# Kernel optimization log

Hardware: AMD Instinct MI355X
Metric: run time of the kernel (lower is better)

## Reference

```python
import jax, jax.numpy as jnp
import numpy as np

B, S, D, H, F = 4, 2048, 512, 8, 2048
HD = D // H
SCALE = HD ** -0.5


def layernorm(x, g, b, eps=1e-5):
    mu = jnp.mean(x, axis=-1, keepdims=True)
    var = jnp.var(x, axis=-1, keepdims=True)
    return (x - mu) * jax.lax.rsqrt(var + eps) * g + b


def setup_inputs() -> dict:
    key = jax.random.key(0)
    ks = jax.random.split(key, 10)
    s = 0.02
    return {
        "x": jax.random.normal(ks[0], (B, S, D), jnp.float32),
        "w_qkv": jax.random.normal(ks[1], (D, 3 * D), jnp.float32) * s,
        "b_qkv": jnp.zeros((3 * D,), jnp.float32),
        "w_o": jax.random.normal(ks[2], (D, D), jnp.float32) * s,
        "b_o": jnp.zeros((D,), jnp.float32),
        "w1": jax.random.normal(ks[3], (D, F), jnp.float32) * s,
        "b1": jnp.zeros((F,), jnp.float32),
        "w2": jax.random.normal(ks[4], (F, D), jnp.float32) * s,
        "b2": jnp.zeros((D,), jnp.float32),
        "g1": jnp.ones((D,), jnp.float32),
        "be1": jnp.zeros((D,), jnp.float32),
        "g2": jnp.ones((D,), jnp.float32),
        "be2": jnp.zeros((D,), jnp.float32),
    }


def reference(x, w_qkv, b_qkv, w_o, b_o, w1, b1, w2, b2, g1, be1, g2, be2):
    res = x
    qkv = x @ w_qkv + b_qkv                       # [B,S,3D]
    q, k, v = jnp.split(qkv, 3, axis=-1)          # each [B,S,D]
    # head partition: [B,S,D] -> [B,H,S,hd]
    def split_heads(t):
        return t.reshape(B, S, H, HD).transpose(0, 2, 1, 3)
    q, k, v = map(split_heads, (q, k, v))
    scores = jnp.einsum('bhqc,bhkc->bhqk', q, k) * SCALE
    weights = jax.nn.softmax(scores, axis=-1)
    out = jnp.einsum('bhqk,bhkc->bhqc', weights, v)
    out = out.transpose(0, 2, 1, 3).reshape(B, S, D)  # merge heads
    out = out @ w_o + b_o
    out = layernorm(out + res, g1, be1)
    res = out
    out = jax.nn.gelu(out @ w1 + b1, approximate=False) @ w2 + b2
    out = layernorm(out + res, g2, be2)
    return out
```

## Files before the change

### kernel.cpp

```cpp
#include <hip/hip_runtime.h>
#include <math.h>

constexpr int B = 4, S = 2048, D = 512, H = 8, HD = 64, F = 2048;
constexpr int M = B * S;
constexpr float C_QK = 0.125f * 1.44269504088896340736f;

typedef __bf16 bf16x8 __attribute__((ext_vector_type(8)));
typedef float  f32x4  __attribute__((ext_vector_type(4)));
typedef float  f32x16 __attribute__((ext_vector_type(16)));

static __device__ __forceinline__ short f2bf(float f) {
  return __builtin_bit_cast(short, (__bf16)f);
}

static __device__ __forceinline__ void gload16(const void* g, void* l) {
  __builtin_amdgcn_global_load_lds(
      (const __attribute__((address_space(1))) unsigned int*)g,
      (__attribute__((address_space(3))) unsigned int*)l, 16, 0, 0);
}

__global__ __launch_bounds__(256)
void cast_x(const float4* __restrict__ in, short4* __restrict__ out) {
  int i = blockIdx.x * 256 + threadIdx.x;
  float4 v = in[i];
  out[i] = make_short4(f2bf(v.x), f2bf(v.y), f2bf(v.z), f2bf(v.w));
}

__global__ __launch_bounds__(256)
void tcast(const float* __restrict__ in, short* __restrict__ out, int R, int C) {
  __shared__ float tl[32][33];
  const int t = threadIdx.x;
  const int r0 = blockIdx.y * 32, c0 = blockIdx.x * 32;
  const int tr = t >> 3, tc4 = (t & 7) * 4;
  float4 v = *(const float4*)&in[(size_t)(r0 + tr) * C + c0 + tc4];
  tl[tr][tc4] = v.x; tl[tr][tc4 + 1] = v.y; tl[tr][tc4 + 2] = v.z; tl[tr][tc4 + 3] = v.w;
  __syncthreads();
  short4 o = make_short4(f2bf(tl[tc4][tr]), f2bf(tl[tc4 + 1][tr]),
                         f2bf(tl[tc4 + 2][tr]), f2bf(tl[tc4 + 3][tr]));
  *(short4*)&out[(size_t)(c0 + tr) * R + r0 + tc4] = o;
}

template<int BM, int GELU, int EPI>
__global__ __launch_bounds__(256)
void gemm_bf16(const short* __restrict__ A, const short* __restrict__ Wt,
               const float* __restrict__ bias,
               float* __restrict__ Cf, short* __restrict__ Cb,
               short* __restrict__ qsw, short* __restrict__ ksw,
               short* __restrict__ vsw, int K, int N) {
  constexpr int MI = BM / 32;
  __shared__ short As[BM * 32] __attribute__((aligned(16)));
  __shared__ short Bs[128 * 32] __attribute__((aligned(16)));
  const int t = threadIdx.x;
  const int w = t >> 6, l = t & 63, g = l >> 4, r = l & 15;
  const int wm = w >> 1, wn = w & 1;
  const int m0 = blockIdx.y * BM, n0 = blockIdx.x * 128;
  f32x4 acc[MI][4] = {};
  for (int k0 = 0; k0 < K; k0 += 32) {
    __syncthreads();
#pragma unroll
    for (int iss = 0; iss < BM / 64; ++iss) {
      int q = iss * 256 + t;
      gload16(A + (size_t)(m0 + (q >> 2)) * K + k0 + (q & 3) * 8, (char*)As + q * 16);
    }
#pragma unroll
    for (int iss = 0; iss < 2; ++iss) {
      int q = iss * 256 + t;
      gload16(Wt + (size_t)(n0 + (q >> 2)) * K + k0 + (q & 3) * 8, (char*)Bs + q * 16);
    }
    __syncthreads();
    bf16x8 aF[MI], bF[4];
#pragma unroll
    for (int mi = 0; mi < MI; ++mi)
      aF[mi] = *(const bf16x8*)(As + (wm * (MI * 16) + mi * 16 + r) * 32 + g * 8);
#pragma unroll
    for (int ni = 0; ni < 4; ++ni)
      bF[ni] = *(const bf16x8*)(Bs + (wn * 64 + ni * 16 + r) * 32 + g * 8);
#pragma unroll
    for (int mi = 0; mi < MI; ++mi)
#pragma unroll
      for (int ni = 0; ni < 4; ++ni)
        acc[mi][ni] = __builtin_amdgcn_mfma_f32_16x16x32_bf16(aF[mi], bF[ni], acc[mi][ni], 0, 0, 0);
  }
#pragma unroll
  for (int mi = 0; mi < MI; ++mi) {
#pragma unroll
    for (int ni = 0; ni < 4; ++ni) {
      const int n  = n0 + wn * 64 + ni * 16 + r;
      const int mB = m0 + wm * (MI * 16) + mi * 16 + g * 4;
      float vals[4];
#pragma unroll
      for (int j = 0; j < 4; ++j) {
        float v = acc[mi][ni][j] + bias[n];
        if (GELU) v = 0.5f * v * (1.0f + erff(v * 0.70710678118654752f));
        vals[j] = v;
      }
      if (EPI == 0) {
#pragma unroll
        for (int j = 0; j < 4; ++j) Cf[(size_t)(mB + j) * N + n] = vals[j];
      } else if (EPI == 1) {
#pragma unroll
        for (int j = 0; j < 4; ++j) Cb[(size_t)(mB + j) * N + n] = f2bf(vals[j]);
      } else {
        const int b = mB >> 11, s = mB & 2047;
        if (n < 512) {
          const int hh = n >> 6, d = n & 63;
          const size_t rb = (size_t)(b * 8 + hh) * 2048;
#pragma unroll
          for (int j = 0; j < 4; ++j)
            qsw[(rb + s + j) * 64 + (d ^ (((s + j) & 7) << 3))] = f2bf(vals[j] * C_QK);
        } else if (n < 1024) {
          const int hh = (n - 512) >> 6, d = (n - 512) & 63;
          const size_t rb = (size_t)(b * 8 + hh) * 2048;
#pragma unroll
          for (int j = 0; j < 4; ++j)
            ksw[(rb + s + j) * 64 + (d ^ (((s + j) & 7) << 3))] = f2bf(vals[j]);
        } else {
          const int hh = (n - 1024) >> 6, d = (n - 1024) & 63;
          short4 pk = make_short4(f2bf(vals[0]), f2bf(vals[1]), f2bf(vals[2]), f2bf(vals[3]));
          *(short4*)&vsw[(size_t)((b * 8 + hh) * 64 + d) * 2048 + (s ^ ((d & 7) << 3))] = pk;
        }
      }
    }
  }
}

__global__ __launch_bounds__(256)
void attn_mfma(const short* __restrict__ qsw, const short* __restrict__ ksw,
               const short* __restrict__ vsw, short* __restrict__ attn_o) {
  __shared__ short Qs[128 * 64] __attribute__((aligned(16)));
  __shared__ short Ks[64 * 64] __attribute__((aligned(16)));
  __shared__ short Vs[64 * 64] __attribute__((aligned(16)));
  const int t = threadIdx.x;
  const int w = t >> 6, l = t & 63;
  const int c = l & 31, hi = l >> 5;
  const int bh = blockIdx.y;
  const int q0 = blockIdx.x * 128;
  const short* qb = qsw + ((size_t)bh * 2048 + q0) * 64;
  const short* kb = ksw + (size_t)bh * 2048 * 64;
  const short* vb = vsw + (size_t)bh * 64 * 2048;

#pragma unroll
  for (int iss = 0; iss < 4; ++iss) {
    int q = iss * 256 + t;
    gload16(qb + (q >> 3) * 64 + (q & 7) * 8, (char*)Qs + q * 16);
  }
  __syncthreads();
  const int qrow = w * 32 + c;
  const int swz = (c & 7) << 3;
  bf16x8 qf[4];
#pragma unroll
  for (int dc = 0; dc < 4; ++dc)
    qf[dc] = *(const bf16x8*)(Qs + qrow * 64 + ((dc * 16 + hi * 8) ^ swz));

  f32x16 o0 = {}, o1 = {};
  float m_run = -3e38f, l_run = 0.0f;

  for (int kt = 0; kt < S; kt += 64) {
    __syncthreads();
#pragma unroll
    for (int iss = 0; iss < 2; ++iss) {
      int q = iss * 256 + t;
      gload16(kb + (size_t)(kt + (q >> 3)) * 64 + (q & 7) * 8, (char*)Ks + q * 16);
    }
#pragma unroll
    for (int iss = 0; iss < 2; ++iss) {
      int q = iss * 256 + t;
      gload16(vb + (size_t)(q >> 3) * 2048 + kt + (q & 7) * 8, (char*)Vs + q * 16);
    }
    __syncthreads();

    f32x16 s0 = {}, s1 = {};
#pragma unroll
    for (int dc = 0; dc < 4; ++dc) {
      const int koff = (dc * 16 + hi * 8) ^ swz;
      bf16x8 kf0 = *(const bf16x8*)(Ks + c * 64 + koff);
      bf16x8 kf1 = *(const bf16x8*)(Ks + (32 + c) * 64 + koff);
      s0 = __builtin_amdgcn_mfma_f32_32x32x16_bf16(kf0, qf[dc], s0, 0, 0, 0);
      s1 = __builtin_amdgcn_mfma_f32_32x32x16_bf16(kf1, qf[dc], s1, 0, 0, 0);
    }
    float tmax = -3e38f;
#pragma unroll
    for (int j = 0; j < 16; ++j) tmax = fmaxf(tmax, fmaxf(s0[j], s1[j]));
    tmax = fmaxf(tmax, __shfl_xor(tmax, 32, 64));
    if (__any(tmax - m_run > 8.0f)) {
      float mnew = fmaxf(m_run, tmax);
      float rs = __builtin_amdgcn_exp2f(m_run - mnew);
      m_run = mnew;
      l_run *= rs;
#pragma unroll
      for (int j = 0; j < 16; ++j) {
        float rj = __shfl(rs, (j & 3) + 8 * (j >> 2) + 4 * hi, 64);
        o0[j] *= rj; o1[j] *= rj;
      }
    }
    float rsum = 0.0f;
#pragma unroll
    for (int j = 0; j < 16; ++j) {
      s0[j] = __builtin_amdgcn_exp2f(s0[j] - m_run);
      s1[j] = __builtin_amdgcn_exp2f(s1[j] - m_run);
      rsum += s0[j] + s1[j];
    }
    rsum += __shfl_xor(rsum, 32, 64);
    l_run += rsum;

#pragma unroll
    for (int kc = 0; kc < 4; ++kc) {
      const int jb = (kc & 1) * 8;
      int u0, u1, v0, v1;
      if (kc < 2) {
        asm("v_cvt_pk_bf16_f32 %0, %1, %2" : "=v"(u0) : "v"(s0[jb + 0]), "v"(s0[jb + 1]));
        asm("v_cvt_pk_bf16_f32 %0, %1, %2" : "=v"(u1) : "v"(s0[jb + 2]), "v"(s0[jb + 3]));
        asm("v_cvt_pk_bf16_f32 %0, %1, %2" : "=v"(v0) : "v"(s0[jb + 4]), "v"(s0[jb + 5]));
        asm("v_cvt_pk_bf16_f32 %0, %1, %2" : "=v"(v1) : "v"(s0[jb + 6]), "v"(s0[jb + 7]));
      } else {
        asm("v_cvt_pk_bf16_f32 %0, %1, %2" : "=v"(u0) : "v"(s1[jb + 0]), "v"(s1[jb + 1]));
        asm("v_cvt_pk_bf16_f32 %0, %1, %2" : "=v"(u1) : "v"(s1[jb + 2]), "v"(s1[jb + 3]));
        asm("v_cvt_pk_bf16_f32 %0, %1, %2" : "=v"(v0) : "v"(s1[jb + 4]), "v"(s1[jb + 5]));
        asm("v_cvt_pk_bf16_f32 %0, %1, %2" : "=v"(v1) : "v"(s1[jb + 6]), "v"(s1[jb + 7]));
      }
      asm volatile("v_permlane32_swap_b32 %0, %1" : "+v"(u0), "+v"(v0));
      asm volatile("v_permlane32_swap_b32 %0, %1" : "+v"(u1), "+v"(v1));
      int pw[4] = {u0, u1, v0, v1};
      bf16x8 pa = __builtin_bit_cast(bf16x8, *(int4*)pw);
      const int voff = (kc * 16 + hi * 8) ^ swz;
      bf16x8 vf0 = *(const bf16x8*)(Vs + c * 64 + voff);
      bf16x8 vf1 = *(const bf16x8*)(Vs + (32 + c) * 64 + voff);
      o0 = __builtin_amdgcn_mfma_f32_32x32x16_bf16(pa, vf0, o0, 0, 0, 0);
      o1 = __builtin_amdgcn_mfma_f32_32x32x16_bf16(pa, vf1, o1, 0, 0, 0);
    }
  }
  const int b = bh >> 3, hh = bh & 7;
  float inv = 1.0f / l_run;
#pragma unroll
  for (int j = 0; j < 16; ++j) {
    const int q_rel = (j & 3) + 8 * (j >> 2) + 4 * hi;
    float invq = __shfl(inv, q_rel, 64);
    const size_t row = (size_t)(b * 2048 + q0 + w * 32 + q_rel) * 512 + hh * 64;
    attn_o[row + c]      = f2bf(o0[j] * invq);
    attn_o[row + 32 + c] = f2bf(o1[j] * invq);
  }
}

template<int WB>
__global__ __launch_bounds__(256)
void add_ln(const float* __restrict__ a, const float* __restrict__ res,
            const float* __restrict__ g_, const float* __restrict__ be,
            float* __restrict__ out, short* __restrict__ outb) {
  const int row = blockIdx.x;
  const int t = threadIdx.x;
  const size_t off = (size_t)row * D;
  float x0 = a[off + t] + res[off + t];
  float x1 = a[off + t + 256] + res[off + t + 256];
  float sum = x0 + x1;
  float sq  = x0 * x0 + x1 * x1;
#pragma unroll
  for (int o2 = 32; o2 > 0; o2 >>= 1) {
    sum += __shfl_down(sum, o2);
    sq  += __shfl_down(sq, o2);
  }
  __shared__ float ssum[4], ssq[4];
  const int wid = t >> 6;
  if ((t & 63) == 0) { ssum[wid] = sum; ssq[wid] = sq; }
  __syncthreads();
  if (t == 0) {
    ssum[0] = ssum[0] + ssum[1] + ssum[2] + ssum[3];
    ssq[0]  = ssq[0] + ssq[1] + ssq[2] + ssq[3];
  }
  __syncthreads();
  float mu   = ssum[0] * (1.0f / D);
  float var  = ssq[0] * (1.0f / D) - mu * mu;
  float rstd = rsqrtf(var + 1e-5f);
  float y0 = (x0 - mu) * rstd * g_[t] + be[t];
  float y1 = (x1 - mu) * rstd * g_[t + 256] + be[t + 256];
  out[off + t] = y0;
  out[off + t + 256] = y1;
  if (WB) {
    outb[off + t] = f2bf(y0);
    outb[off + t + 256] = f2bf(y1);
  }
}

extern "C" void kernel_launch(void* const* d_in, const int* in_sizes, int n_in,
                              void* d_out, int out_size, void* d_ws, size_t ws_size,
                              hipStream_t stream) {
  const float* x     = (const float*)d_in[0];
  const float* w_qkv = (const float*)d_in[1];
  const float* b_qkv = (const float*)d_in[2];
  const float* w_o   = (const float*)d_in[3];
  const float* b_o   = (const float*)d_in[4];
  const float* w1    = (const float*)d_in[5];
  const float* b1    = (const float*)d_in[6];
  const float* w2    = (const float*)d_in[7];
  const float* b2    = (const float*)d_in[8];
  const float* g1    = (const float*)d_in[9];
  const float* be1   = (const float*)d_in[10];
  const float* g2    = (const float*)d_in[11];
  const float* be2   = (const float*)d_in[12];
  float* out = (float*)d_out;
  (void)in_sizes; (void)n_in; (void)out_size; (void)ws_size;

  const size_t MD = (size_t)M * 512;
  short* q_sw = (short*)d_ws;
  short* k_sw = q_sw + MD;
  short* v_sw = k_sw + MD;
  short* a_o  = v_sw + MD;
  short* h    = q_sw;
  short* xb   = a_o + MD;
  short* ln1b = xb;
  short* wtq  = xb + MD;
  short* wto  = wtq + (size_t)1536 * 512;
  short* wt1  = wto + (size_t)512 * 512;
  short* wt2  = wt1 + (size_t)512 * 2048;
  float* buf  = (float*)(wt2 + (size_t)2048 * 512);
  float* ln1  = buf + MD;

  cast_x<<<4096, 256, 0, stream>>>((const float4*)x, (short4*)xb);
  tcast<<<dim3(48, 16), 256, 0, stream>>>(w_qkv, wtq, 512, 1536);
  tcast<<<dim3(16, 16), 256, 0, stream>>>(w_o,  wto, 512, 512);
  tcast<<<dim3(64, 16), 256, 0, stream>>>(w1,   wt1, 512, 2048);
  tcast<<<dim3(16, 64), 256, 0, stream>>>(w2,   wt2, 2048, 512);

  gemm_bf16<128, 0, 2><<<dim3(12, 64), 256, 0, stream>>>(
      xb, wtq, b_qkv, nullptr, nullptr, q_sw, k_sw, v_sw, 512, 1536);
  attn_mfma<<<dim3(16, 32), 256, 0, stream>>>(q_sw, k_sw, v_sw, a_o);
  gemm_bf16<128, 0, 0><<<dim3(4, 64), 256, 0, stream>>>(
      a_o, wto, b_o, buf, nullptr, nullptr, nullptr, nullptr, 512, 512);
  add_ln<1><<<M, 256, 0, stream>>>(buf, x, g1, be1, ln1, ln1b);
  gemm_bf16<128, 1, 1><<<dim3(16, 64), 256, 0, stream>>>(
      ln1b, wt1, b1, nullptr, h, nullptr, nullptr, nullptr, 512, 2048);
  gemm_bf16<128, 0, 0><<<dim3(4, 64), 256, 0, stream>>>(
      h, wt2, b2, buf, nullptr, nullptr, nullptr, nullptr, 2048, 512);
  add_ln<0><<<M, 256, 0, stream>>>(buf, ln1, g2, be2, out, nullptr);
}
```

Measured before the change: 305.7 us.

## Double-buffer GEMM and attention LDS tiles, fuse prep casts into one kernel

```diff
diff --git a/kernel.cpp b/kernel.cpp
--- a/kernel.cpp
+++ b/kernel.cpp
@@ -20,17 +20,26 @@
 }
 
 __global__ __launch_bounds__(256)
-void cast_x(const float4* __restrict__ in, short4* __restrict__ out) {
-  int i = blockIdx.x * 256 + threadIdx.x;
-  float4 v = in[i];
-  out[i] = make_short4(f2bf(v.x), f2bf(v.y), f2bf(v.z), f2bf(v.w));
-}
-
-__global__ __launch_bounds__(256)
-void tcast(const float* __restrict__ in, short* __restrict__ out, int R, int C) {
+void prep_all(const float* __restrict__ x, short* __restrict__ xb,
+              const float* __restrict__ w_qkv, short* __restrict__ wtq,
+              const float* __restrict__ w_o,  short* __restrict__ wto,
+              const float* __restrict__ w1,   short* __restrict__ wt1,
+              const float* __restrict__ w2,   short* __restrict__ wt2) {
   __shared__ float tl[32][33];
+  const int id = blockIdx.x;
   const int t = threadIdx.x;
-  const int r0 = blockIdx.y * 32, c0 = blockIdx.x * 32;
+  if (id < 4096) {
+    int i = id * 256 + t;
+    float4 v = ((const float4*)x)[i];
+    ((short4*)xb)[i] = make_short4(f2bf(v.x), f2bf(v.y), f2bf(v.z), f2bf(v.w));
+    return;
+  }
+  const float* in; short* out; int R, C, bx, by;
+  if (id < 4864)      { int k = id - 4096; in = w_qkv; out = wtq; R = 512;  C = 1536; bx = k % 48; by = k / 48; }
+  else if (id < 5120) { int k = id - 4864; in = w_o;   out = wto; R = 512;  C = 512;  bx = k % 16; by = k / 16; }
+  else if (id < 6144) { int k = id - 5120; in = w1;    out = wt1; R = 512;  C = 2048; bx = k % 64; by = k / 64; }
+  else                { int k = id - 6144; in = w2;    out = wt2; R = 2048; C = 512;  bx = k % 16; by = k / 16; }
+  const int r0 = by * 32, c0 = bx * 32;
   const int tr = t >> 3, tc4 = (t & 7) * 4;
   float4 v = *(const float4*)&in[(size_t)(r0 + tr) * C + c0 + tc4];
   tl[tr][tc4] = v.x; tl[tr][tc4 + 1] = v.y; tl[tr][tc4 + 2] = v.z; tl[tr][tc4 + 3] = v.w;
@@ -40,53 +49,77 @@
   *(short4*)&out[(size_t)(c0 + tr) * R + r0 + tc4] = o;
 }
 
-template<int BM, int GELU, int EPI>
+template<int GELU, int EPI>
 __global__ __launch_bounds__(256)
 void gemm_bf16(const short* __restrict__ A, const short* __restrict__ Wt,
                const float* __restrict__ bias,
                float* __restrict__ Cf, short* __restrict__ Cb,
                short* __restrict__ qsw, short* __restrict__ ksw,
                short* __restrict__ vsw, int K, int N) {
-  constexpr int MI = BM / 32;
-  __shared__ short As[BM * 32] __attribute__((aligned(16)));
-  __shared__ short Bs[128 * 32] __attribute__((aligned(16)));
+  __shared__ short As[2][128 * 64] __attribute__((aligned(16)));
+  __shared__ short Bs[2][128 * 64] __attribute__((aligned(16)));
   const int t = threadIdx.x;
   const int w = t >> 6, l = t & 63, g = l >> 4, r = l & 15;
   const int wm = w >> 1, wn = w & 1;
-  const int m0 = blockIdx.y * BM, n0 = blockIdx.x * 128;
-  f32x4 acc[MI][4] = {};
-  for (int k0 = 0; k0 < K; k0 += 32) {
+  const int m0 = blockIdx.y * 128, n0 = blockIdx.x * 128;
+
+#define STAGE_TILE(buf, k0)                                                     \
+  {                                                                             \
+    _Pragma("unroll")                                                           \
+    for (int iss = 0; iss < 4; ++iss) {                                         \
+      int q = iss * 256 + t;                                                    \
+      int row = q >> 3, sl = (q & 7) ^ (row & 7);                               \
+      gload16(A + (size_t)(m0 + row) * K + (k0) + sl * 8,                       \
+              (char*)As[buf] + q * 16);                                         \
+    }                                                                           \
+    _Pragma("unroll")                                                           \
+    for (int iss = 0; iss < 4; ++iss) {                                         \
+      int q = iss * 256 + t;                                                    \
+      int row = q >> 3, sl = (q & 7) ^ (row & 7);                               \
+      gload16(Wt + (size_t)(n0 + row) * K + (k0) + sl * 8,                      \
+              (char*)Bs[buf] + q * 16);                                         \
+    }                                                                           \
+  }
+
+  f32x4 acc[4][4] = {};
+  const int NS = K >> 6;
+  STAGE_TILE(0, 0);
+  __syncthreads();
+  for (int st = 0; st < NS; ++st) {
+    const int cur = st & 1;
+    if (st + 1 < NS) STAGE_TILE(cur ^ 1, (st + 1) << 6);
+    const short* Ac = As[cur];
+    const short* Bc = Bs[cur];
+#pragma unroll
+    for (int kh = 0; kh < 2; ++kh) {
+      const int cc = kh * 4 + g;
+      bf16x8 aF[4], bF[4];
+#pragma unroll
+      for (int mi = 0; mi < 4; ++mi) {
+        const int row = wm * 64 + mi * 16 + r;
+        aF[mi] = *(const bf16x8*)(Ac + row * 64 + ((cc ^ (r & 7)) << 3));
+      }
+#pragma unroll
+      for (int ni = 0; ni < 4; ++ni) {
+        const int row = wn * 64 + ni * 16 + r;
+        bF[ni] = *(const bf16x8*)(Bc + row * 64 + ((cc ^ (r & 7)) << 3));
+      }
+#pragma unroll
+      for (int mi = 0; mi < 4; ++mi)
+#pragma unroll
+        for (int ni = 0; ni < 4; ++ni)
+          acc[mi][ni] = __builtin_amdgcn_mfma_f32_16x16x32_bf16(aF[mi], bF[ni], acc[mi][ni], 0, 0, 0);
+    }
     __syncthreads();
-#pragma unroll
-    for (int iss = 0; iss < BM / 64; ++iss) {
-      int q = iss * 256 + t;
-      gload16(A + (size_t)(m0 + (q >> 2)) * K + k0 + (q & 3) * 8, (char*)As + q * 16);
-    }
-#pragma unroll
-    for (int iss = 0; iss < 2; ++iss) {
-      int q = iss * 256 + t;
-      gload16(Wt + (size_t)(n0 + (q >> 2)) * K + k0 + (q & 3) * 8, (char*)Bs + q * 16);
-    }
-    __syncthreads();
-    bf16x8 aF[MI], bF[4];
-#pragma unroll
-    for (int mi = 0; mi < MI; ++mi)
-      aF[mi] = *(const bf16x8*)(As + (wm * (MI * 16) + mi * 16 + r) * 32 + g * 8);
-#pragma unroll
-    for (int ni = 0; ni < 4; ++ni)
-      bF[ni] = *(const bf16x8*)(Bs + (wn * 64 + ni * 16 + r) * 32 + g * 8);
-#pragma unroll
-    for (int mi = 0; mi < MI; ++mi)
-#pragma unroll
-      for (int ni = 0; ni < 4; ++ni)
-        acc[mi][ni] = __builtin_amdgcn_mfma_f32_16x16x32_bf16(aF[mi], bF[ni], acc[mi][ni], 0, 0, 0);
-  }
-#pragma unroll
-  for (int mi = 0; mi < MI; ++mi) {
+  }
+#undef STAGE_TILE
+
+#pragma unroll
+  for (int mi = 0; mi < 4; ++mi) {
 #pragma unroll
     for (int ni = 0; ni < 4; ++ni) {
       const int n  = n0 + wn * 64 + ni * 16 + r;
-      const int mB = m0 + wm * (MI * 16) + mi * 16 + g * 4;
+      const int mB = m0 + wm * 64 + mi * 16 + g * 4;
       float vals[4];
 #pragma unroll
       for (int j = 0; j < 4; ++j) {
@@ -128,8 +161,8 @@
 void attn_mfma(const short* __restrict__ qsw, const short* __restrict__ ksw,
                const short* __restrict__ vsw, short* __restrict__ attn_o) {
   __shared__ short Qs[128 * 64] __attribute__((aligned(16)));
-  __shared__ short Ks[64 * 64] __attribute__((aligned(16)));
-  __shared__ short Vs[64 * 64] __attribute__((aligned(16)));
+  __shared__ short Ks[2][64 * 64] __attribute__((aligned(16)));
+  __shared__ short Vs[2][64 * 64] __attribute__((aligned(16)));
   const int t = threadIdx.x;
   const int w = t >> 6, l = t & 63;
   const int c = l & 31, hi = l >> 5;
@@ -139,12 +172,30 @@
   const short* kb = ksw + (size_t)bh * 2048 * 64;
   const short* vb = vsw + (size_t)bh * 64 * 2048;
 
+#define STAGE_KV(buf, kt)                                                       \
+  {                                                                             \
+    _Pragma("unroll")                                                           \
+    for (int iss = 0; iss < 2; ++iss) {                                         \
+      int q = iss * 256 + t;                                                    \
+      gload16(kb + (size_t)((kt) + (q >> 3)) * 64 + (q & 7) * 8,                \
+              (char*)Ks[buf] + q * 16);                                         \
+    }                                                                           \
+    _Pragma("unroll")                                                           \
+    for (int iss = 0; iss < 2; ++iss) {                                         \
+      int q = iss * 256 + t;                                                    \
+      gload16(vb + (size_t)(q >> 3) * 2048 + (kt) + (q & 7) * 8,                \
+              (char*)Vs[buf] + q * 16);                                         \
+    }                                                                           \
+  }
+
 #pragma unroll
   for (int iss = 0; iss < 4; ++iss) {
     int q = iss * 256 + t;
     gload16(qb + (q >> 3) * 64 + (q & 7) * 8, (char*)Qs + q * 16);
   }
-  __syncthreads();
+  STAGE_KV(0, 0);
+  __syncthreads();
+
   const int qrow = w * 32 + c;
   const int swz = (c & 7) << 3;
   bf16x8 qf[4];
@@ -155,29 +206,24 @@
   f32x16 o0 = {}, o1 = {};
   float m_run = -3e38f, l_run = 0.0f;
 
-  for (int kt = 0; kt < S; kt += 64) {
-    __syncthreads();
-#pragma unroll
-    for (int iss = 0; iss < 2; ++iss) {
-      int q = iss * 256 + t;
-      gload16(kb + (size_t)(kt + (q >> 3)) * 64 + (q & 7) * 8, (char*)Ks + q * 16);
-    }
-#pragma unroll
-    for (int iss = 0; iss < 2; ++iss) {
-      int q = iss * 256 + t;
-      gload16(vb + (size_t)(q >> 3) * 2048 + kt + (q & 7) * 8, (char*)Vs + q * 16);
-    }
-    __syncthreads();
+  for (int ti = 0; ti < 32; ++ti) {
+    const int cur = ti & 1;
+    if (ti < 31) STAGE_KV(cur ^ 1, (ti + 1) * 64);
+    const short* Kc = Ks[cur];
+    const short* Vc = Vs[cur];
 
     f32x16 s0 = {}, s1 = {};
+    __builtin_amdgcn_s_setprio(1);
 #pragma unroll
     for (int dc = 0; dc < 4; ++dc) {
       const int koff = (dc * 16 + hi * 8) ^ swz;
-      bf16x8 kf0 = *(const bf16x8*)(Ks + c * 64 + koff);
-      bf16x8 kf1 = *(const bf16x8*)(Ks + (32 + c) * 64 + koff);
+      bf16x8 kf0 = *(const bf16x8*)(Kc + c * 64 + koff);
+      bf16x8 kf1 = *(const bf16x8*)(Kc + (32 + c) * 64 + koff);
       s0 = __builtin_amdgcn_mfma_f32_32x32x16_bf16(kf0, qf[dc], s0, 0, 0, 0);
       s1 = __builtin_amdgcn_mfma_f32_32x32x16_bf16(kf1, qf[dc], s1, 0, 0, 0);
     }
+    __builtin_amdgcn_s_setprio(0);
+
     float tmax = -3e38f;
 #pragma unroll
     for (int j = 0; j < 16; ++j) tmax = fmaxf(tmax, fmaxf(s0[j], s1[j]));
@@ -203,6 +249,7 @@
     rsum += __shfl_xor(rsum, 32, 64);
     l_run += rsum;
 
+    __builtin_amdgcn_s_setprio(1);
 #pragma unroll
     for (int kc = 0; kc < 4; ++kc) {
       const int jb = (kc & 1) * 8;
@@ -223,12 +270,16 @@
       int pw[4] = {u0, u1, v0, v1};
       bf16x8 pa = __builtin_bit_cast(bf16x8, *(int4*)pw);
       const int voff = (kc * 16 + hi * 8) ^ swz;
-      bf16x8 vf0 = *(const bf16x8*)(Vs + c * 64 + voff);
-      bf16x8 vf1 = *(const bf16x8*)(Vs + (32 + c) * 64 + voff);
+      bf16x8 vf0 = *(const bf16x8*)(Vc + c * 64 + voff);
+      bf16x8 vf1 = *(const bf16x8*)(Vc + (32 + c) * 64 + voff);
       o0 = __builtin_amdgcn_mfma_f32_32x32x16_bf16(pa, vf0, o0, 0, 0, 0);
       o1 = __builtin_amdgcn_mfma_f32_32x32x16_bf16(pa, vf1, o1, 0, 0, 0);
     }
-  }
+    __builtin_amdgcn_s_setprio(0);
+    __syncthreads();
+  }
+#undef STAGE_KV
+
   const int b = bh >> 3, hh = bh & 7;
   float inv = 1.0f / l_run;
 #pragma unroll
@@ -314,21 +365,17 @@
   float* buf  = (float*)(wt2 + (size_t)2048 * 512);
   float* ln1  = buf + MD;
 
-  cast_x<<<4096, 256, 0, stream>>>((const float4*)x, (short4*)xb);
-  tcast<<<dim3(48, 16), 256, 0, stream>>>(w_qkv, wtq, 512, 1536);
-  tcast<<<dim3(16, 16), 256, 0, stream>>>(w_o,  wto, 512, 512);
-  tcast<<<dim3(64, 16), 256, 0, stream>>>(w1,   wt1, 512, 2048);
-  tcast<<<dim3(16, 64), 256, 0, stream>>>(w2,   wt2, 2048, 512);
-
-  gemm_bf16<128, 0, 2><<<dim3(12, 64), 256, 0, stream>>>(
+  prep_all<<<7168, 256, 0, stream>>>(x, xb, w_qkv, wtq, w_o, wto, w1, wt1, w2, wt2);
+
+  gemm_bf16<0, 2><<<dim3(12, 64), 256, 0, stream>>>(
       xb, wtq, b_qkv, nullptr, nullptr, q_sw, k_sw, v_sw, 512, 1536);
   attn_mfma<<<dim3(16, 32), 256, 0, stream>>>(q_sw, k_sw, v_sw, a_o);
-  gemm_bf16<128, 0, 0><<<dim3(4, 64), 256, 0, stream>>>(
+  gemm_bf16<0, 0><<<dim3(4, 64), 256, 0, stream>>>(
       a_o, wto, b_o, buf, nullptr, nullptr, nullptr, nullptr, 512, 512);
   add_ln<1><<<M, 256, 0, stream>>>(buf, x, g1, be1, ln1, ln1b);
-  gemm_bf16<128, 1, 1><<<dim3(16, 64), 256, 0, stream>>>(
+  gemm_bf16<1, 1><<<dim3(16, 64), 256, 0, stream>>>(
       ln1b, wt1, b1, nullptr, h, nullptr, nullptr, nullptr, 512, 2048);
-  gemm_bf16<128, 0, 0><<<dim3(4, 64), 256, 0, stream>>>(
+  gemm_bf16<0, 0><<<dim3(4, 64), 256, 0, stream>>>(
       h, wt2, b2, buf, nullptr, nullptr, nullptr, nullptr, 2048, 512);
   add_ln<0><<<M, 256, 0, stream>>>(buf, ln1, g2, be2, out, nullptr);
 }
```

Measured after the change: 294.8 us. -3.6%, faster.
